# Performance work log

Measured on AMD Instinct MI355X. Metric: run time of the kernel, lower is better.

The kernel has to match this reference:

```python
import jax, jax.numpy as jnp
from jax import lax
import numpy as np

N, E, L, H, B, R = 12800, 204800, 24, 128, 64, 8
VN, VA = 100, 20


def _p(key, *shape):
    return jax.random.normal(key, shape, dtype=jnp.float32) * 0.05


def setup_inputs() -> dict:
    key = jax.random.key(0)
    ks = jax.random.split(key, 32)
    inp = {
        'nodeTypes': jax.random.randint(ks[0], (N,), 0, VN),
        'edge_index': jax.random.randint(ks[1], (2, E), 0, N),
        'edge_attr': jax.random.randint(ks[2], (E,), 0, R),
        'bs': jnp.repeat(jnp.arange(B, dtype=jnp.int32), N // B),
        'sequence_input': jax.random.uniform(ks[3], (N, L), dtype=jnp.float32),
        'nodes_bs': jnp.full((B,), N // B, dtype=jnp.int32),
        'len_seq': jnp.full((B,), L, dtype=jnp.int32),
        'action_input': jax.random.randint(ks[4], (B,), 0, VA),
        # parameters (RGCN weights SHARED across the 2 layers, as in the source)
        'emb_nodes_w': _p(ks[5], VN, H),
        'emb_actions_w': _p(ks[6], VA, H),
        'rgcn_W': _p(ks[7], R, H, H),
        'rgcn_root': _p(ks[8], H, H),
        'rgcn_b': _p(ks[9], H),
        'gru_Wih': _p(ks[10], 3 * H, H),
        'gru_Whh': _p(ks[11], 3 * H, H),
        'gru_bih': _p(ks[12], 3 * H),
        'gru_bhh': _p(ks[13], 3 * H),
        'linA_w': _p(ks[14], H, H),
        'linA_b': _p(ks[15], H),
        'linAf_w': _p(ks[16], VA, H),
        'linAf_b': _p(ks[17], VA),
        'linN_w': _p(ks[18], H, 2 * H),
        'linN_b': _p(ks[19], H),
        'linNf_w': _p(ks[20], 1, H),
        'linNf_b': _p(ks[21], 1),
        'fin_w': _p(ks[22], H, H),
        'fin_b': _p(ks[23], H),
        'finf_w': _p(ks[24], 1, H),
        'finf_b': _p(ks[25], 1),
    }
    return inp


def _rgcn(x, src, dst, etype, W, Wroot, b):
    # PyG RGCNConv: per-relation mean aggregation, then per-relation weight, plus root + bias
    comb = dst * R + etype  # combined (node, relation) segment id
    msg = jax.ops.segment_sum(x[src], comb, num_segments=N * R)  # [N*R, H]
    cnt = jax.ops.segment_sum(jnp.ones((src.shape[0],), x.dtype), comb, num_segments=N * R)
    mean = (msg / jnp.maximum(cnt, 1.0)[:, None]).reshape(N, R, H)
    return jnp.einsum('nrh,rhd->nd', mean, W) + x @ Wroot + b


def _gru(x_seq, h0, Wih, Whh, bih, bhh):
    # torch GRU gate order: r, z, n ; x_seq [B, T, H]
    def step(h, x):
        gi = x @ Wih.T + bih
        gh = h @ Whh.T + bhh
        i_r, i_z, i_n = jnp.split(gi, 3, axis=-1)
        h_r, h_z, h_n = jnp.split(gh, 3, axis=-1)
        r = jax.nn.sigmoid(i_r + h_r)
        z = jax.nn.sigmoid(i_z + h_z)
        n = jnp.tanh(i_n + r * h_n)
        h_new = (1.0 - z) * n + z * h
        return h_new, h_new
    _, ys = lax.scan(step, h0, jnp.swapaxes(x_seq, 0, 1))
    return jnp.swapaxes(ys, 0, 1)


def _seg_softmax(x, seg, nseg):
    m = jax.ops.segment_max(x, seg, num_segments=nseg)
    e = jnp.exp(x - m[seg])
    s = jax.ops.segment_sum(e, seg, num_segments=nseg)
    return e / s[seg]


def reference(nodeTypes, edge_index, edge_attr, bs, sequence_input, nodes_bs, len_seq,
              action_input, emb_nodes_w, emb_actions_w, rgcn_W, rgcn_root, rgcn_b,
              gru_Wih, gru_Whh, gru_bih, gru_bhh, linA_w, linA_b, linAf_w, linAf_b,
              linN_w, linN_b, linNf_w, linNf_b, fin_w, fin_b, finf_w, finf_b):
    src, dst = edge_index[0], edge_index[1]
    x = emb_nodes_w[nodeTypes]
    for _ in range(2):  # shared-weight RGCN layers + ReLU
        x = jax.nn.relu(_rgcn(x, src, dst, edge_attr, rgcn_W, rgcn_root, rgcn_b))
    nodeEmb = x  # [N, H]

    cnt = jax.ops.segment_sum(jnp.ones((N,), x.dtype), bs, num_segments=B)
    h_G = jax.ops.segment_sum(nodeEmb, bs, num_segments=B) / cnt[:, None]  # [B, H]

    action = jax.nn.relu(h_G @ linA_w.T + linA_b) @ linAf_w.T + linAf_b  # [B, VA]
    final = jax.nn.sigmoid(jax.nn.relu(h_G @ fin_w.T + fin_b) @ finf_w.T + finf_b)  # [B, 1]

    sos = emb_actions_w[action_input][:, None, :]  # [B, 1, H]
    # scatter-sum of per-timestep weighted node embeddings -> [B, L, H]
    emb_seq = sequence_input[:, :, None] * nodeEmb[:, None, :]  # [N, L, H]
    agg = jax.ops.segment_sum(emb_seq, bs, num_segments=B)
    input_gru = jnp.concatenate([sos, agg], axis=1)[:, :L]  # len_seq == L drops last step
    seq = _gru(input_gru, h_G, gru_Wih, gru_Whh, gru_bih, gru_bhh)  # [B, L, H]

    # linNodes(cat(out_gru, nodeEmb)) computed without materializing the [N,L,2H] concat
    part1 = jnp.einsum('blh,oh->blo', seq, linN_w[:, :H])[bs]      # [N, L, H]
    part2 = nodeEmb @ linN_w[:, H:].T                               # [N, H]
    hidden = jax.nn.relu(part1 + part2[:, None, :] + linN_b)       # [N, L, H]
    logits = jnp.einsum('nlh,h->nl', hidden, linNf_w[0]) + linNf_b[0]  # [N, L]
    nodes_final = _seg_softmax(logits, bs, B)
    return (action, nodes_final, final)
```

## Files before the change

kernel.cpp:

```cpp
#include <hip/hip_runtime.h>
#include <math.h>

#define NN 12800
#define NE 204800
#define LL 24
#define HH 128
#define BB 64
#define RR 8
#define VAx 20
#define KC 1152
#define CHK 8
#define PS 16

typedef __attribute__((ext_vector_type(8))) short bf16x8;
typedef __attribute__((ext_vector_type(4))) float f32x4;

__device__ inline unsigned short f2bf(float f) {
  unsigned u = __float_as_uint(f);
  unsigned r = u + 0x7FFF + ((u >> 16) & 1);
  return (unsigned short)(r >> 16);
}
__device__ inline float bf2f(unsigned short s) {
  return __uint_as_float(((unsigned)s) << 16);
}
__device__ inline unsigned packbf(float lo, float hi) {
  return (unsigned)f2bf(lo) | ((unsigned)f2bf(hi) << 16);
}

__global__ void k_prep(const float* __restrict__ rgcnW, const float* __restrict__ rgcnRoot,
                       unsigned short* __restrict__ wcatT,
                       const float* __restrict__ linN_w, unsigned short* __restrict__ linN2bt,
                       const float* __restrict__ Wih, unsigned short* __restrict__ Wihbt,
                       const float* __restrict__ Whh, float* __restrict__ WhhT,
                       const float* __restrict__ linA_w, float* __restrict__ linAT,
                       const float* __restrict__ fin_w, float* __restrict__ finT,
                       unsigned short* __restrict__ linN1bt,
                       const int* __restrict__ nt, const float* __restrict__ embN,
                       unsigned int* __restrict__ x, int* __restrict__ deg) {
  int idx = blockIdx.x * 256 + threadIdx.x;
  if (idx < HH * KC) {
    int d = idx / KC, k = idx - d * KC;
    float v = (k < 1024) ? rgcnW[(k >> 7) * (HH * HH) + (k & 127) * HH + d]
                         : rgcnRoot[(k - 1024) * HH + d];
    wcatT[idx] = f2bf(v);
    return;
  }
  idx -= HH * KC;
  if (idx < HH * HH) {
    int d = idx >> 7, k = idx & 127;
    linN2bt[idx] = f2bf(linN_w[d * 2 * HH + HH + k]);
    return;
  }
  idx -= HH * HH;
  if (idx < 3 * HH * HH) {
    Wihbt[idx] = f2bf(Wih[idx]);
    return;
  }
  idx -= 3 * HH * HH;
  if (idx < 3 * HH * HH) {
    int r = idx / HH, c = idx - r * HH;
    WhhT[c * 384 + r] = Whh[r * HH + c];
    return;
  }
  idx -= 3 * HH * HH;
  if (idx < HH * HH) {
    int r = idx >> 7, c = idx & 127;
    linAT[c * HH + r] = linA_w[r * HH + c];
    return;
  }
  idx -= HH * HH;
  if (idx < HH * HH) {
    int r = idx >> 7, c = idx & 127;
    finT[c * HH + r] = fin_w[r * HH + c];
    return;
  }
  idx -= HH * HH;
  if (idx < HH * HH) {
    int o = idx >> 7, k = idx & 127;
    linN1bt[idx] = f2bf(linN_w[o * 2 * HH + k]);
    return;
  }
  idx -= HH * HH;
  if (idx < NN * 64) {
    int n = idx >> 6, p = idx & 63;
    const float* e = embN + (size_t)nt[n] * HH + p * 2;
    x[idx] = packbf(e[0], e[1]);
    return;
  }
  idx -= NN * 64;
  if (idx < NN * PS) deg[idx] = 0;
}
#define PREP_TOTAL (HH * KC + HH * HH + 3 * HH * HH + 3 * HH * HH + HH * HH + HH * HH + HH * HH + NN * 64 + NN * PS)

__global__ void k_count(const int* __restrict__ edst, int* __restrict__ deg,
                        const int* __restrict__ bs, int* __restrict__ bptr) {
  int i = blockIdx.x * 256 + threadIdx.x;
  if (i < NE) atomicAdd(&deg[edst[i] * PS], 1);
  if (i < NN) {
    int b = bs[i];
    if (i == 0 || bs[i - 1] != b) bptr[b] = i;
    if (i == NN - 1) bptr[BB] = NN;
  }
}

__global__ __launch_bounds__(1024) void k_scane(const int* __restrict__ deg,
                                                int* __restrict__ indptr,
                                                int* __restrict__ cur) {
  __shared__ int ws[16];
  int tid = threadIdx.x;
  const int per = (NN + 1023) >> 10;
  int i0 = tid * per;
  int s = 0;
  for (int k = 0; k < per; ++k) {
    int i = i0 + k;
    if (i < NN) s += deg[i * PS];
  }
  int lane = tid & 63, wv = tid >> 6;
  int incl = s;
#pragma unroll
  for (int off = 1; off < 64; off <<= 1) {
    int t = __shfl_up(incl, off);
    if (lane >= off) incl += t;
  }
  if (lane == 63) ws[wv] = incl;
  __syncthreads();
  if (tid < 16) {
    int v = ws[tid];
    int inc = v;
#pragma unroll
    for (int off = 1; off < 16; off <<= 1) {
      int t = __shfl_up(inc, off);
      if (tid >= off) inc += t;
    }
    ws[tid] = inc - v;
  }
  __syncthreads();
  int run = ws[wv] + incl - s;
  for (int k = 0; k < per; ++k) {
    int i = i0 + k;
    if (i < NN) {
      indptr[i] = run;
      cur[i * PS] = run;
      run += deg[i * PS];
      if (i == NN - 1) indptr[NN] = run;
    }
  }
}

__global__ void k_scattere(const int* __restrict__ esrc, const int* __restrict__ edst,
                           const int* __restrict__ erel, int* __restrict__ cur,
                           int* __restrict__ esort) {
  int i = blockIdx.x * 256 + threadIdx.x;
  if (i >= NE) return;
  int p = atomicAdd(&cur[edst[i] * PS], 1);
  esort[p] = esrc[i] | (erel[i] << 16);
}

__global__ __launch_bounds__(256) void k_agg(const unsigned int* __restrict__ x,
                                             const int* __restrict__ indptr,
                                             const int* __restrict__ esort,
                                             unsigned int* __restrict__ A, int n0, int nc) {
  int wid = ((blockIdx.x * 256) + threadIdx.x) >> 6;
  int lane = threadIdx.x & 63;
  if (wid >= nc) return;
  int n = n0 + wid;
  float a0=0,a1=0,a2=0,a3=0,a4=0,a5=0,a6=0,a7=0;
  float b0=0,b1=0,b2=0,b3=0,b4=0,b5=0,b6=0,b7=0;
  int c0=0,c1=0,c2=0,c3=0,c4=0,c5=0,c6=0,c7=0;
  int e0 = indptr[n], e1 = indptr[n + 1];

#define ACCV(RV, VV)                                                              \
  {                                                                               \
    float v0_ = bf2f((unsigned short)((VV) & 0xFFFF));                            \
    float v1_ = bf2f((unsigned short)((VV) >> 16));                               \
    switch (RV) {                                                                 \
      case 0: a0 += v0_; b0 += v1_; c0++; break;                                  \
      case 1: a1 += v0_; b1 += v1_; c1++; break;                                  \
      case 2: a2 += v0_; b2 += v1_; c2++; break;                                  \
      case 3: a3 += v0_; b3 += v1_; c3++; break;                                  \
      case 4: a4 += v0_; b4 += v1_; c4++; break;                                  \
      case 5: a5 += v0_; b5 += v1_; c5++; break;                                  \
      case 6: a6 += v0_; b6 += v1_; c6++; break;                                  \
      default: a7 += v0_; b7 += v1_; c7++; break;                                 \
    }                                                                             \
  }

  int e = e0;
  for (; e + 8 <= e1; e += 8) {
    int pk0 = esort[e + 0], pk1 = esort[e + 1], pk2 = esort[e + 2], pk3 = esort[e + 3];
    int pk4 = esort[e + 4], pk5 = esort[e + 5], pk6 = esort[e + 6], pk7 = esort[e + 7];
    unsigned v0 = x[(size_t)(pk0 & 0xFFFF) * 64 + lane];
    unsigned v1 = x[(size_t)(pk1 & 0xFFFF) * 64 + lane];
    unsigned v2 = x[(size_t)(pk2 & 0xFFFF) * 64 + lane];
    unsigned v3 = x[(size_t)(pk3 & 0xFFFF) * 64 + lane];
    unsigned v4 = x[(size_t)(pk4 & 0xFFFF) * 64 + lane];
    unsigned v5 = x[(size_t)(pk5 & 0xFFFF) * 64 + lane];
    unsigned v6 = x[(size_t)(pk6 & 0xFFFF) * 64 + lane];
    unsigned v7 = x[(size_t)(pk7 & 0xFFFF) * 64 + lane];
    ACCV(pk0 >> 16, v0);
    ACCV(pk1 >> 16, v1);
    ACCV(pk2 >> 16, v2);
    ACCV(pk3 >> 16, v3);
    ACCV(pk4 >> 16, v4);
    ACCV(pk5 >> 16, v5);
    ACCV(pk6 >> 16, v6);
    ACCV(pk7 >> 16, v7);
  }
  for (; e + 4 <= e1; e += 4) {
    int pk0 = esort[e + 0], pk1 = esort[e + 1], pk2 = esort[e + 2], pk3 = esort[e + 3];
    unsigned v0 = x[(size_t)(pk0 & 0xFFFF) * 64 + lane];
    unsigned v1 = x[(size_t)(pk1 & 0xFFFF) * 64 + lane];
    unsigned v2 = x[(size_t)(pk2 & 0xFFFF) * 64 + lane];
    unsigned v3 = x[(size_t)(pk3 & 0xFFFF) * 64 + lane];
    ACCV(pk0 >> 16, v0);
    ACCV(pk1 >> 16, v1);
    ACCV(pk2 >> 16, v2);
    ACCV(pk3 >> 16, v3);
  }
  for (; e < e1; ++e) {
    int pk = esort[e];
    unsigned v = x[(size_t)(pk & 0xFFFF) * 64 + lane];
    ACCV(pk >> 16, v);
  }
#undef ACCV

  unsigned int* Ar = A + (size_t)wid * (KC / 2);
  float i0 = 1.0f / (float)(c0 > 0 ? c0 : 1);
  float i1 = 1.0f / (float)(c1 > 0 ? c1 : 1);
  float i2 = 1.0f / (float)(c2 > 0 ? c2 : 1);
  float i3 = 1.0f / (float)(c3 > 0 ? c3 : 1);
  float i4 = 1.0f / (float)(c4 > 0 ? c4 : 1);
  float i5 = 1.0f / (float)(c5 > 0 ? c5 : 1);
  float i6 = 1.0f / (float)(c6 > 0 ? c6 : 1);
  float i7 = 1.0f / (float)(c7 > 0 ? c7 : 1);
  Ar[0 * 64 + lane] = packbf(a0 * i0, b0 * i0);
  Ar[1 * 64 + lane] = packbf(a1 * i1, b1 * i1);
  Ar[2 * 64 + lane] = packbf(a2 * i2, b2 * i2);
  Ar[3 * 64 + lane] = packbf(a3 * i3, b3 * i3);
  Ar[4 * 64 + lane] = packbf(a4 * i4, b4 * i4);
  Ar[5 * 64 + lane] = packbf(a5 * i5, b5 * i5);
  Ar[6 * 64 + lane] = packbf(a6 * i6, b6 * i6);
  Ar[7 * 64 + lane] = packbf(a7 * i7, b7 * i7);
  Ar[512 + lane] = x[n * 64 + lane];
}

template <int OUTMODE>
__global__ __launch_bounds__(256) void k_mgemm(const unsigned short* __restrict__ Abf, int lda,
                                               const unsigned short* __restrict__ BTbf, int ldb,
                                               const float* __restrict__ bias,
                                               void* __restrict__ C, int ldc, int M, int K) {
  __shared__ unsigned int ldsu[(8192 + 16384) / 4];
  char* ldsc = (char*)ldsu;
  int tid = threadIdx.x;
  int m0 = blockIdx.x * 64;
  int n0c = blockIdx.y * 128;
  int w = tid >> 6, l = tid & 63;
  int lrow = l & 15, lg = l >> 4;
  f32x4 acc[8] = {};

  const char* Ab = (const char*)Abf;
  const char* Bb = (const char*)(BTbf + (size_t)n0c * ldb);
  int KT = K >> 6;
  for (int kt = 0; kt < KT; ++kt) {
    int k0 = kt << 6;
#pragma unroll
    for (int i = 0; i < 2; ++i) {
      int slot = i * 256 + tid;
      int row = slot >> 3;
      int colb = (slot & 7) << 4;
      int gr = m0 + row;
      gr = gr < M ? gr : M - 1;
      size_t srcb = ((size_t)gr * lda + k0) * 2 + (size_t)(colb ^ ((row & 7) << 4));
      __builtin_amdgcn_global_load_lds((const unsigned int*)(Ab + srcb),
                                       (unsigned int*)(ldsc + slot * 16), 16, 0, 0);
    }
#pragma unroll
    for (int i = 0; i < 4; ++i) {
      int slot = i * 256 + tid;
      int row = slot >> 3;
      int colb = (slot & 7) << 4;
      size_t srcb = ((size_t)row * ldb + k0) * 2 + (size_t)(colb ^ ((row & 7) << 4));
      __builtin_amdgcn_global_load_lds((const unsigned int*)(Bb + srcb),
                                       (unsigned int*)(ldsc + 8192 + slot * 16), 16, 0, 0);
    }
    __syncthreads();
#pragma unroll
    for (int h = 0; h < 2; ++h) {
      int arow = w * 16 + lrow;
      bf16x8 af = *(const bf16x8*)(ldsc + arow * 128 +
                                   ((h * 64 + lg * 16) ^ ((arow & 7) << 4)));
#pragma unroll
      for (int c = 0; c < 8; ++c) {
        int brow = c * 16 + lrow;
        bf16x8 bf = *(const bf16x8*)(ldsc + 8192 + brow * 128 +
                                     ((h * 64 + lg * 16) ^ ((brow & 7) << 4)));
        acc[c] = __builtin_amdgcn_mfma_f32_16x16x32_bf16(af, bf, acc[c], 0, 0, 0);
      }
    }
    __syncthreads();
  }
#pragma unroll
  for (int c = 0; c < 8; ++c) {
#pragma unroll
    for (int r = 0; r < 4; ++r) {
      int gm = m0 + w * 16 + lg * 4 + r;
      if (gm >= M) continue;
      int gn = n0c + c * 16 + lrow;
      float v = acc[c][r];
      if (OUTMODE == 1) {
        v = fmaxf(v + bias[gn], 0.f);
        ((unsigned short*)C)[(size_t)gm * ldc + gn] = f2bf(v);
      } else if (OUTMODE == 2) {
        ((float*)C)[(size_t)gm * ldc + gn] = v + bias[gn];
      } else {
        ((float*)C)[(size_t)gm * ldc + gn] = v;
      }
    }
  }
}

__global__ __launch_bounds__(256) void k_aggS_part(const float* __restrict__ seqin,
                                                   const unsigned short* __restrict__ x,
                                                   const int* __restrict__ bptr,
                                                   float* __restrict__ part) {
  int bc = blockIdx.x, b = bc >> 3, c = bc & 7;
  int h = threadIdx.x & 127, l0 = threadIdx.x >> 7;
  int i0 = bptr[b], i1 = bptr[b + 1];
  int len = i1 - i0;
  int per = (len + CHK - 1) / CHK;
  int j0 = i0 + c * per;
  int j1 = j0 + per;
  if (j1 > i1) j1 = i1;
  float acc[12] = {};
  float esum = 0.f;
  for (int n = j0; n < j1; ++n) {
    float e = bf2f(x[n * HH + h]);
    esum += e;
    const float* srow = seqin + (size_t)n * LL;
#pragma unroll
    for (int t = 0; t < 12; ++t) acc[t] = fmaf(srow[l0 + 2 * t], e, acc[t]);
  }
  float* p = part + (size_t)bc * 25 * HH + h;
#pragma unroll
  for (int t = 0; t < 12; ++t) p[(l0 + 2 * t) * HH] = acc[t];
  if (l0 == 0) p[24 * HH] = esum;
}

__global__ void k_aggS_red(const float* __restrict__ part, const int* __restrict__ bptr,
                           const float* __restrict__ embA, const int* __restrict__ act,
                           unsigned short* __restrict__ ig, float* __restrict__ hG) {
  int idx = blockIdx.x * 256 + threadIdx.x;
  if (idx >= BB * 25 * HH) return;
  int h = idx & 127;
  int rem = idx >> 7;
  int l = rem % 25, b = rem / 25;
  if (l == 23) {
    ig[((size_t)b * LL) * HH + h] = f2bf(embA[(size_t)act[b] * HH + h]);
    return;
  }
  float s = 0.f;
#pragma unroll
  for (int c = 0; c < CHK; ++c) s += part[(((size_t)(b * CHK + c)) * 25 + l) * HH + h];
  if (l == 24) {
    int len = bptr[b + 1] - bptr[b];
    hG[b * HH + h] = s / (float)len;
  } else {
    ig[((size_t)b * LL + l + 1) * HH + h] = f2bf(s);
  }
}

__global__ __launch_bounds__(128) void k_heads(const float* __restrict__ hG,
                                               const float* __restrict__ linAT,
                                               const float* __restrict__ linA_b,
                                               const float* __restrict__ linAf_w,
                                               const float* __restrict__ linAf_b,
                                               const float* __restrict__ finT,
                                               const float* __restrict__ fin_b,
                                               const float* __restrict__ finf_w,
                                               const float* __restrict__ finf_b,
                                               float* __restrict__ outA,
                                               float* __restrict__ outF) {
  int b = blockIdx.x >> 1, which = blockIdx.x & 1, j = threadIdx.x;
  __shared__ float hsh[HH], t1[HH];
  hsh[j] = hG[b * HH + j];
  __syncthreads();
  const float* Wt = which ? finT : linAT;
  const float* bb = which ? fin_b : linA_b;
  float s = bb[j];
  for (int k = 0; k < HH; ++k) s = fmaf(hsh[k], Wt[k * HH + j], s);
  t1[j] = fmaxf(s, 0.f);
  __syncthreads();
  if (which == 0) {
    if (j < VAx) {
      float o = linAf_b[j];
      for (int k = 0; k < HH; ++k) o = fmaf(t1[k], linAf_w[j * HH + k], o);
      outA[b * VAx + j] = o;
    }
  } else if (j == 0) {
    float o = finf_b[0];
    for (int k = 0; k < HH; ++k) o = fmaf(t1[k], finf_w[k], o);
    outF[b] = 1.f / (1.f + expf(-o));
  }
}

__global__ __launch_bounds__(384) void k_gru(const float* __restrict__ gi,
                                             const float* __restrict__ WhhT,
                                             const float* __restrict__ bhh,
                                             const float* __restrict__ hG,
                                             unsigned short* __restrict__ seqout) {
  int b = blockIdx.x, tid = threadIdx.x;
  int gate = tid >> 7, j = tid & 127;
  __shared__ float h[HH];
  __shared__ float sz[HH], sg[HH];
  float w[HH];
#pragma unroll
  for (int k = 0; k < HH; ++k) w[k] = WhhT[k * 384 + tid];
  float bh = bhh[tid];
  if (tid < HH) h[tid] = hG[b * HH + tid];
  __syncthreads();
  const float* gib = gi + (size_t)b * LL * 384;
  for (int t = 0; t < LL; ++t) {
    float giv = gib[t * 384 + tid];
    float gin = (gate == 0) ? gib[t * 384 + 256 + j] : 0.f;
    float hj = h[j];
    float g0 = 0.f, g1 = 0.f, g2 = 0.f, g3 = 0.f;
    const float4* h4 = (const float4*)h;
#pragma unroll
    for (int k4 = 0; k4 < HH / 4; ++k4) {
      float4 hv = h4[k4];
      g0 = fmaf(w[4 * k4 + 0], hv.x, g0);
      g1 = fmaf(w[4 * k4 + 1], hv.y, g1);
      g2 = fmaf(w[4 * k4 + 2], hv.z, g2);
      g3 = fmaf(w[4 * k4 + 3], hv.w, g3);
    }
    float g = bh + ((g0 + g1) + (g2 + g3));
    float r = 0.f;
    if (gate == 0) {
      r = 1.f / (1.f + expf(-(giv + g)));
    } else if (gate == 1) {
      sz[j] = 1.f / (1.f + expf(-(giv + g)));
    } else {
      sg[j] = g;
    }
    __syncthreads();
    if (gate == 0) {
      float n = tanhf(gin + r * sg[j]);
      float z = sz[j];
      float hn = (1.f - z) * n + z * hj;
      h[j] = hn;
      seqout[((size_t)b * LL + t) * HH + j] = f2bf(hn);
    }
    __syncthreads();
  }
}

__global__ __launch_bounds__(256) void k_logits(const float* __restrict__ part1,
                                                const float* __restrict__ part2,
                                                const float* __restrict__ linN_b,
                                                const float* __restrict__ linNf_w,
                                                const float* __restrict__ linNf_b,
                                                const int* __restrict__ bs,
                                                float* __restrict__ logits) {
  int wid = ((blockIdx.x * 256) + threadIdx.x) >> 6;
  int lane = threadIdx.x & 63;
  if (wid >= NN) return;
  int n = wid;
  int b = bs[n];
  float p2a = part2[n * HH + lane] + linN_b[lane];
  float p2b = part2[n * HH + 64 + lane] + linN_b[64 + lane];
  float wa = linNf_w[lane], wb = linNf_w[64 + lane];
  const float* p1 = part1 + (size_t)b * LL * HH;
  float bf = linNf_b[0];
  for (int l = 0; l < LL; ++l) {
    float v = fmaxf(p1[l * HH + lane] + p2a, 0.f) * wa +
              fmaxf(p1[l * HH + 64 + lane] + p2b, 0.f) * wb;
#pragma unroll
    for (int off = 32; off > 0; off >>= 1) v += __shfl_down(v, off);
    if (lane == 0) logits[n * LL + l] = v + bf;
  }
}

__global__ __launch_bounds__(64) void k_softmax(const float* __restrict__ logits,
                                                const int* __restrict__ bptr,
                                                float* __restrict__ outN) {
  int b = blockIdx.x / LL, l = blockIdx.x % LL;
  int lane = threadIdx.x;
  int i0 = bptr[b], i1 = bptr[b + 1];
  float m = -1e30f;
  for (int i = i0 + lane; i < i1; i += 64) m = fmaxf(m, logits[i * LL + l]);
#pragma unroll
  for (int off = 32; off > 0; off >>= 1) m = fmaxf(m, __shfl_xor(m, off));
  float s = 0.f;
  for (int i = i0 + lane; i < i1; i += 64) s += expf(logits[i * LL + l] - m);
#pragma unroll
  for (int off = 32; off > 0; off >>= 1) s += __shfl_xor(s, off);
  float inv = 1.f / s;
  for (int i = i0 + lane; i < i1; i += 64) {
    outN[i * LL + l] = expf(logits[i * LL + l] - m) * inv;
  }
}

extern "C" void kernel_launch(void* const* d_in, const int* in_sizes, int n_in,
                              void* d_out, int out_size, void* d_ws, size_t ws_size,
                              hipStream_t stream) {
  const int* nodeTypes = (const int*)d_in[0];
  const int* esrc = (const int*)d_in[1];
  const int* edst = esrc + NE;
  const int* erel = (const int*)d_in[2];
  const int* bs = (const int*)d_in[3];
  const float* seqin = (const float*)d_in[4];
  const int* actin = (const int*)d_in[7];
  const float* embN = (const float*)d_in[8];
  const float* embA = (const float*)d_in[9];
  const float* rgcnW = (const float*)d_in[10];
  const float* rgcnRoot = (const float*)d_in[11];
  const float* rgcnB = (const float*)d_in[12];
  const float* Wih = (const float*)d_in[13];
  const float* Whh = (const float*)d_in[14];
  const float* bih = (const float*)d_in[15];
  const float* bhh = (const float*)d_in[16];
  const float* linA_w = (const float*)d_in[17];
  const float* linA_b = (const float*)d_in[18];
  const float* linAf_w = (const float*)d_in[19];
  const float* linAf_b = (const float*)d_in[20];
  const float* linN_w = (const float*)d_in[21];
  const float* linN_b = (const float*)d_in[22];
  const float* linNf_w = (const float*)d_in[23];
  const float* linNf_b = (const float*)d_in[24];
  const float* fin_w = (const float*)d_in[25];
  const float* fin_b = (const float*)d_in[26];
  const float* finf_w = (const float*)d_in[27];
  const float* finf_b = (const float*)d_in[28];

  float* outA = (float*)d_out;
  float* outNodes = outA + BB * VAx;
  float* outF = outNodes + (size_t)NN * LL;

  char* basep = (char*)d_ws;
  size_t off = 0;
  auto alloc = [&](size_t bytes) -> void* {
    void* p = basep + off;
    off = (off + bytes + 255) & ~(size_t)255;
    return p;
  };

  unsigned int* x = (unsigned int*)alloc(sizeof(unsigned int) * NN * 64);
  unsigned int* x2 = (unsigned int*)alloc(sizeof(unsigned int) * NN * 64);
  float* hG = (float*)alloc(sizeof(float) * BB * HH);
  unsigned short* wcatT = (unsigned short*)alloc(sizeof(unsigned short) * HH * KC);
  unsigned short* linN2bt = (unsigned short*)alloc(sizeof(unsigned short) * HH * HH);
  unsigned short* Wihbt = (unsigned short*)alloc(sizeof(unsigned short) * 3 * HH * HH);
  unsigned short* linN1bt = (unsigned short*)alloc(sizeof(unsigned short) * HH * HH);
  float* WhhT = (float*)alloc(sizeof(float) * HH * 3 * HH);
  float* linAT = (float*)alloc(sizeof(float) * HH * HH);
  float* finT = (float*)alloc(sizeof(float) * HH * HH);
  float* part = (float*)alloc(sizeof(float) * BB * CHK * 25 * HH);
  unsigned short* ig = (unsigned short*)alloc(sizeof(unsigned short) * BB * LL * HH);
  float* gi = (float*)alloc(sizeof(float) * BB * LL * 3 * HH);
  unsigned short* seqb = (unsigned short*)alloc(sizeof(unsigned short) * BB * LL * HH);
  float* part1 = (float*)alloc(sizeof(float) * BB * LL * HH);
  float* part2 = (float*)alloc(sizeof(float) * NN * HH);
  float* logitsB = (float*)alloc(sizeof(float) * NN * LL);
  int* deg = (int*)alloc(sizeof(int) * NN * PS);
  int* cur = (int*)alloc(sizeof(int) * NN * PS);
  int* indptr = (int*)alloc(sizeof(int) * (NN + 1));
  int* esort = (int*)alloc(sizeof(int) * NE);
  int* bptr = (int*)alloc(sizeof(int) * (BB + 1));

  size_t remain = (ws_size > off) ? (ws_size - off) : 0;
  int NCk = NN;
  while ((size_t)NCk * KC * 2 > remain && NCk > 100) NCk >>= 1;
  unsigned int* A = (unsigned int*)alloc((size_t)NCk * (KC / 2) * sizeof(unsigned int));

  k_prep<<<(PREP_TOTAL + 255) / 256, 256, 0, stream>>>(
      rgcnW, rgcnRoot, wcatT, linN_w, linN2bt, Wih, Wihbt, Whh, WhhT, linA_w, linAT,
      fin_w, finT, linN1bt, nodeTypes, embN, x, deg);

  k_count<<<(NE + 255) / 256, 256, 0, stream>>>(edst, deg, bs, bptr);
  k_scane<<<1, 1024, 0, stream>>>(deg, indptr, cur);
  k_scattere<<<(NE + 255) / 256, 256, 0, stream>>>(esrc, edst, erel, cur, esort);

  const unsigned int* xin = x;
  unsigned int* xout = x2;
  for (int layer = 0; layer < 2; ++layer) {
    for (int n0 = 0; n0 < NN; n0 += NCk) {
      int nc = NN - n0 < NCk ? NN - n0 : NCk;
      k_agg<<<(nc + 3) / 4, 256, 0, stream>>>(xin, indptr, esort, A, n0, nc);
      dim3 g((nc + 63) / 64, 1);
      k_mgemm<1><<<g, 256, 0, stream>>>(
          (const unsigned short*)A, KC, wcatT, KC, rgcnB,
          (void*)((unsigned short*)xout + (size_t)n0 * HH), HH, nc, KC);
    }
    const unsigned int* t = xin;
    xin = xout;
    xout = (unsigned int*)t;
  }
  const unsigned short* nodeEmb = (const unsigned short*)xin;

  k_aggS_part<<<BB * CHK, 256, 0, stream>>>(seqin, nodeEmb, bptr, part);
  k_aggS_red<<<(BB * 25 * HH + 255) / 256, 256, 0, stream>>>(part, bptr, embA, actin, ig, hG);

  k_heads<<<2 * BB, HH, 0, stream>>>(hG, linAT, linA_b, linAf_w, linAf_b, finT, fin_b,
                                     finf_w, finf_b, outA, outF);

  {
    dim3 g((BB * LL) / 64, 3);
    k_mgemm<2><<<g, 256, 0, stream>>>(ig, HH, Wihbt, HH, bih, (void*)gi, 3 * HH,
                                      BB * LL, HH);
  }
  k_gru<<<BB, 384, 0, stream>>>(gi, WhhT, bhh, hG, seqb);

  {
    dim3 g((BB * LL) / 64, 1);
    k_mgemm<0><<<g, 256, 0, stream>>>(seqb, HH, linN1bt, HH, nullptr, (void*)part1, HH,
                                      BB * LL, HH);
  }
  {
    dim3 g(NN / 64, 1);
    k_mgemm<0><<<g, 256, 0, stream>>>(nodeEmb, HH, linN2bt, HH, nullptr, (void*)part2, HH,
                                      NN, HH);
  }
  k_logits<<<NN / 4, 256, 0, stream>>>(part1, part2, linN_b, linNf_w, linNf_b, bs, logitsB);
  k_softmax<<<BB * LL, 64, 0, stream>>>(logitsB, bptr, outNodes);
}
```

Baseline: 269.9 us.

## Use 32-row tiles for RGCN GEMM and fuse GRU-input and linN2 GEMMs

The RGCN layer GEMM (K=1152, N=128) gets a specialised kernel with 32-row tiles, so twice as many blocks launch and occupancy on the many CUs improves for the 12800-row problem. The GRU input-projection GEMM and the nodeEmb×linN2 GEMM are independent, so they are merged into one launch that splits work by block index, removing a launch and letting both run concurrently. The risks are that the specialised kernel assumes nc divisible by 32 with no bounds checks, and that smaller tiles reload B more often.

```diff
diff --git a/kernel.cpp b/kernel.cpp
--- a/kernel.cpp
+++ b/kernel.cpp
@@ -244,6 +244,69 @@
   Ar[512 + lane] = x[n * 64 + lane];
 }
 
+__global__ __launch_bounds__(256) void k_mgemm_rg32(const unsigned short* __restrict__ Abf,
+                                                    const unsigned short* __restrict__ BTbf,
+                                                    const float* __restrict__ bias,
+                                                    unsigned short* __restrict__ C) {
+  __shared__ unsigned int ldsu[(4096 + 16384) / 4];
+  char* ldsc = (char*)ldsu;
+  int tid = threadIdx.x;
+  int m0 = blockIdx.x * 32;
+  int w = tid >> 6, l = tid & 63;
+  int lrow = l & 15, lg = l >> 4;
+  int rowg = w & 1, colg = w >> 1;
+  f32x4 acc[4] = {};
+
+  const char* Ab = (const char*)Abf;
+  const char* Bb = (const char*)BTbf;
+  for (int kt = 0; kt < KC / 64; ++kt) {
+    int k0 = kt << 6;
+    {
+      int slot = tid;
+      int row = slot >> 3;
+      int colb = (slot & 7) << 4;
+      size_t srcb = ((size_t)(m0 + row) * KC + k0) * 2 + (size_t)(colb ^ ((row & 7) << 4));
+      __builtin_amdgcn_global_load_lds((const unsigned int*)(Ab + srcb),
+                                       (unsigned int*)(ldsc + slot * 16), 16, 0, 0);
+    }
+#pragma unroll
+    for (int i = 0; i < 4; ++i) {
+      int slot = i * 256 + tid;
+      int row = slot >> 3;
+      int colb = (slot & 7) << 4;
+      size_t srcb = ((size_t)row * KC + k0) * 2 + (size_t)(colb ^ ((row & 7) << 4));
+      __builtin_amdgcn_global_load_lds((const unsigned int*)(Bb + srcb),
+                                       (unsigned int*)(ldsc + 4096 + slot * 16), 16, 0, 0);
+    }
+    __syncthreads();
+#pragma unroll
+    for (int h = 0; h < 2; ++h) {
+      int arow = rowg * 16 + lrow;
+      bf16x8 af = *(const bf16x8*)(ldsc + arow * 128 +
+                                   ((h * 64 + lg * 16) ^ ((arow & 7) << 4)));
+#pragma unroll
+      for (int c = 0; c < 4; ++c) {
+        int brow = (colg * 4 + c) * 16 + lrow;
+        bf16x8 bfr = *(const bf16x8*)(ldsc + 4096 + brow * 128 +
+                                      ((h * 64 + lg * 16) ^ ((brow & 7) << 4)));
+        acc[c] = __builtin_amdgcn_mfma_f32_16x16x32_bf16(af, bfr, acc[c], 0, 0, 0);
+      }
+    }
+    __syncthreads();
+  }
+#pragma unroll
+  for (int c = 0; c < 4; ++c) {
+    int gn = (colg * 4 + c) * 16 + lrow;
+    float bv = bias[gn];
+#pragma unroll
+    for (int r = 0; r < 4; ++r) {
+      int gm = m0 + rowg * 16 + lg * 4 + r;
+      float v = fmaxf(acc[c][r] + bv, 0.f);
+      C[(size_t)gm * HH + gn] = f2bf(v);
+    }
+  }
+}
+
 template <int OUTMODE>
 __global__ __launch_bounds__(256) void k_mgemm(const unsigned short* __restrict__ Abf, int lda,
                                                const unsigned short* __restrict__ BTbf, int ldb,
@@ -315,6 +378,94 @@
       } else {
         ((float*)C)[(size_t)gm * ldc + gn] = v;
       }
+    }
+  }
+}
+
+__global__ __launch_bounds__(256) void k_mgemm_gp(const unsigned short* __restrict__ ig,
+                                                  const unsigned short* __restrict__ Wihbt,
+                                                  const float* __restrict__ bih,
+                                                  float* __restrict__ gi,
+                                                  const unsigned short* __restrict__ nodeEmb,
+                                                  const unsigned short* __restrict__ linN2bt,
+                                                  float* __restrict__ part2) {
+  __shared__ unsigned int ldsu[(8192 + 16384) / 4];
+  char* ldsc = (char*)ldsu;
+  int tid = threadIdx.x;
+  int bid = blockIdx.x;
+  const unsigned short* Abf;
+  const unsigned short* BTbf;
+  const float* bias;
+  float* Cf;
+  int m0, ldc, withbias;
+  const int GIB = (BB * LL / 64) * 3;
+  if (bid < GIB) {
+    int mb = bid / 3, nc = bid % 3;
+    Abf = ig;
+    BTbf = Wihbt + (size_t)(nc * 128) * HH;
+    bias = bih + nc * 128;
+    Cf = gi + nc * 128;
+    m0 = mb * 64;
+    ldc = 3 * HH;
+    withbias = 1;
+  } else {
+    Abf = nodeEmb;
+    BTbf = linN2bt;
+    bias = nullptr;
+    Cf = part2;
+    m0 = (bid - GIB) * 64;
+    ldc = HH;
+    withbias = 0;
+  }
+  int w = tid >> 6, l = tid & 63;
+  int lrow = l & 15, lg = l >> 4;
+  f32x4 acc[8] = {};
+  const char* Ab = (const char*)Abf;
+  const char* Bb = (const char*)BTbf;
+  for (int kt = 0; kt < 2; ++kt) {
+    int k0 = kt << 6;
+#pragma unroll
+    for (int i = 0; i < 2; ++i) {
+      int slot = i * 256 + tid;
+      int row = slot >> 3;
+      int colb = (slot & 7) << 4;
+      size_t srcb = ((size_t)(m0 + row) * HH + k0) * 2 + (size_t)(colb ^ ((row & 7) << 4));
+      __builtin_amdgcn_global_load_lds((const unsigned int*)(Ab + srcb),
+                                       (unsigned int*)(ldsc + slot * 16), 16, 0, 0);
+    }
+#pragma unroll
+    for (int i = 0; i < 4; ++i) {
+      int slot = i * 256 + tid;
+      int row = slot >> 3;
+      int colb = (slot & 7) << 4;
+      size_t srcb = ((size_t)row * HH + k0) * 2 + (size_t)(colb ^ ((row & 7) << 4));
+      __builtin_amdgcn_global_load_lds((const unsigned int*)(Bb + srcb),
+                                       (unsigned int*)(ldsc + 8192 + slot * 16), 16, 0, 0);
+    }
+    __syncthreads();
+#pragma unroll
+    for (int h = 0; h < 2; ++h) {
+      int arow = w * 16 + lrow;
+      bf16x8 af = *(const bf16x8*)(ldsc + arow * 128 +
+                                   ((h * 64 + lg * 16) ^ ((arow & 7) << 4)));
+#pragma unroll
+      for (int c = 0; c < 8; ++c) {
+        int brow = c * 16 + lrow;
+        bf16x8 bfr = *(const bf16x8*)(ldsc + 8192 + brow * 128 +
+                                      ((h * 64 + lg * 16) ^ ((brow & 7) << 4)));
+        acc[c] = __builtin_amdgcn_mfma_f32_16x16x32_bf16(af, bfr, acc[c], 0, 0, 0);
+      }
+    }
+    __syncthreads();
+  }
+#pragma unroll
+  for (int c = 0; c < 8; ++c) {
+    int gn = c * 16 + lrow;
+    float bv = withbias ? bias[gn] : 0.f;
+#pragma unroll
+    for (int r = 0; r < 4; ++r) {
+      int gm = m0 + w * 16 + lg * 4 + r;
+      Cf[(size_t)gm * ldc + gn] = acc[c][r] + bv;
     }
   }
 }
@@ -586,10 +737,9 @@
     for (int n0 = 0; n0 < NN; n0 += NCk) {
       int nc = NN - n0 < NCk ? NN - n0 : NCk;
       k_agg<<<(nc + 3) / 4, 256, 0, stream>>>(xin, indptr, esort, A, n0, nc);
-      dim3 g((nc + 63) / 64, 1);
-      k_mgemm<1><<<g, 256, 0, stream>>>(
-          (const unsigned short*)A, KC, wcatT, KC, rgcnB,
-          (void*)((unsigned short*)xout + (size_t)n0 * HH), HH, nc, KC);
+      k_mgemm_rg32<<<nc / 32, 256, 0, stream>>>(
+          (const unsigned short*)A, wcatT, rgcnB,
+          (unsigned short*)xout + (size_t)n0 * HH);
     }
     const unsigned int* t = xin;
     xin = xout;
@@ -600,14 +750,12 @@
   k_aggS_part<<<BB * CHK, 256, 0, stream>>>(seqin, nodeEmb, bptr, part);
   k_aggS_red<<<(BB * 25 * HH + 255) / 256, 256, 0, stream>>>(part, bptr, embA, actin, ig, hG);
 
+  k_mgemm_gp<<<(BB * LL / 64) * 3 + NN / 64, 256, 0, stream>>>(ig, Wihbt, bih, gi,
+                                                               nodeEmb, linN2bt, part2);
+
   k_heads<<<2 * BB, HH, 0, stream>>>(hG, linAT, linA_b, linAf_w, linAf_b, finT, fin_b,
                                      finf_w, finf_b, outA, outF);
 
-  {
-    dim3 g((BB * LL) / 64, 3);
-    k_mgemm<2><<<g, 256, 0, stream>>>(ig, HH, Wihbt, HH, bih, (void*)gi, 3 * HH,
-                                      BB * LL, HH);
-  }
   k_gru<<<BB, 384, 0, stream>>>(gi, WhhT, bhh, hG, seqb);
 
   {
@@ -615,11 +763,6 @@
     k_mgemm<0><<<g, 256, 0, stream>>>(seqb, HH, linN1bt, HH, nullptr, (void*)part1, HH,
                                       BB * LL, HH);
   }
-  {
-    dim3 g(NN / 64, 1);
-    k_mgemm<0><<<g, 256, 0, stream>>>(nodeEmb, HH, linN2bt, HH, nullptr, (void*)part2, HH,
-                                      NN, HH);
-  }
   k_logits<<<NN / 4, 256, 0, stream>>>(part1, part2, linN_b, linNf_w, linNf_b, bs, logitsB);
   k_softmax<<<BB * LL, 64, 0, stream>>>(logitsB, bptr, outNodes);
 }
```

Measured after the change: 248.5 us. 1.09x faster.
